# Kernel optimization log

Hardware: AMD Instinct MI355X
Metric: run time of the kernel (lower is better)

## Reference

```python
import jax, jax.numpy as jnp
import numpy as np

NUM_HEADS = 6

def setup_inputs() -> dict:
    key = jax.random.key(0)
    ks = jax.random.split(key, 6)
    B_, N, C = 4096, 64, 192
    nW = 4096
    return {
        "x": jax.random.normal(ks[0], (B_, N, C), dtype=jnp.float32),
        "mask": jax.random.normal(ks[1], (nW, N, N), dtype=jnp.float32),
        "qkv_w": jax.random.normal(ks[2], (3 * C, C), dtype=jnp.float32) * 0.02,
        "qkv_b": jax.random.normal(ks[3], (3 * C,), dtype=jnp.float32) * 0.02,
        "proj_w": jax.random.normal(ks[4], (C, C), dtype=jnp.float32) * 0.02,
        "proj_b": jax.random.normal(ks[5], (C,), dtype=jnp.float32) * 0.02,
    }

def reference(x, mask, qkv_w, qkv_b, proj_w, proj_b):
    B_, N, C = x.shape
    H = NUM_HEADS
    hd = C // H
    scale = hd ** -0.5
    qkv = (x @ qkv_w.T + qkv_b).reshape(B_, N, 3, H, hd)
    qkv = jnp.transpose(qkv, (2, 0, 3, 1, 4))  # [3, B_, H, N, hd]
    q, k, v = qkv[0], qkv[1], qkv[2]
    attn = jnp.einsum('bhnd,bhmd->bhnm', q * scale, k)  # [B_, H, N, N]
    nW = mask.shape[0]
    # additive relative/shift mask broadcast over image batch and heads
    attn = attn.reshape(B_ // nW, nW, H, N, N) + mask[None, :, None, :, :]
    attn = attn.reshape(B_, H, N, N)
    attn = jax.nn.softmax(attn, axis=-1)
    out = jnp.einsum('bhnm,bhmd->bhnd', attn, v)  # [B_, H, N, hd]
    out = jnp.transpose(out, (0, 2, 1, 3)).reshape(B_, N, C)
    return out @ proj_w.T + proj_b
```

## Files before the change

kernel.cpp:

```cpp
#include <hip/hip_runtime.h>
#include <stdint.h>


#define NTOK 64
#define CDIM 192
#define KROW 40
#define VROW 72

#define WS_KV 36864
#define WS_P  110592

typedef __attribute__((ext_vector_type(4))) float f32x4;
typedef __attribute__((ext_vector_type(8))) short bf16x8;

__device__ __forceinline__ short f2bf(float f) {
  union { float f; uint32_t u; } v; v.f = f;
  return (short)(uint16_t)((v.u + 0x7FFFu + ((v.u >> 16) & 1u)) >> 16);
}
__device__ __forceinline__ uint32_t pack2(float a, float b) {
  return (uint32_t)(uint16_t)f2bf(a) | ((uint32_t)(uint16_t)f2bf(b) << 16);
}

__device__ __forceinline__ bf16x8 xpose(uint32_t A0, uint32_t A1,
                                        uint32_t B0, uint32_t B1,
                                        int s0, int s1, int hiSel) {
  uint32_t w[4];
  uint32_t a, b;
  a = (uint32_t)__shfl((int)A0, s0); b = (uint32_t)__shfl((int)B0, s0); w[0] = hiSel ? b : a;
  a = (uint32_t)__shfl((int)A1, s0); b = (uint32_t)__shfl((int)B1, s0); w[1] = hiSel ? b : a;
  a = (uint32_t)__shfl((int)A0, s1); b = (uint32_t)__shfl((int)B0, s1); w[2] = hiSel ? b : a;
  a = (uint32_t)__shfl((int)A1, s1); b = (uint32_t)__shfl((int)B1, s1); w[3] = hiSel ? b : a;
  return *reinterpret_cast<bf16x8*>(w);
}

#define GLOAD16(g, l) __builtin_amdgcn_global_load_lds( \
    (const __attribute__((address_space(1))) void*)(g), \
    (__attribute__((address_space(3))) void*)(l), 16, 0, 0)

__global__ void wconv_kernel(const float* __restrict__ qkv_w,
                             const float* __restrict__ proj_w,
                             short* __restrict__ ws) {
  const int r = blockIdx.x, c = threadIdx.x;
  float val;
  int base, lr;
  if (r < 192) {
    base = (r >> 6) * 12288; lr = r & 63;
    val = qkv_w[r * CDIM + c];
  } else if (r < 576) {
    const int rr = r - 192;
    const int h = (rr % 192) >> 5;
    lr = rr & 31;
    base = WS_KV + h * 12288 + ((rr < 192) ? 0 : 6144);
    val = qkv_w[r * CDIM + c];
  } else {
    const int rr = r - 576;
    base = WS_P + (rr >> 6) * 12288; lr = rr & 63;
    val = proj_w[rr * CDIM + c];
  }
  const int s = c >> 3, lo = c & 7;
  const int sp = (s & 24) | ((s ^ lr) & 7);
  ws[base + lr * CDIM + sp * 8 + lo] = f2bf(val);
}

__device__ __forceinline__ void stage_issue(short* __restrict__ wbuf,
                                            const short* __restrict__ src, int tid) {
  const int w = tid >> 6, lane = tid & 63;
  #pragma unroll
  for (int it = 0; it < 6; ++it) {
    const int cidx = it * 4 + w;
    GLOAD16(src + cidx * 512 + lane * 8, wbuf + cidx * 512);
  }
}

__global__ __launch_bounds__(256, 4)
void winattn_kernel(const float* __restrict__ x, const float* __restrict__ mask,
                    const short* __restrict__ ws,
                    const float* __restrict__ qkv_b, const float* __restrict__ proj_b,
                    float* __restrict__ out) {
  __shared__ __align__(16) short wbuf[64 * CDIM];
  __shared__ __align__(16) short kh[NTOK * KROW];
  __shared__ __align__(16) short vth[32 * VROW];

  const int b    = blockIdx.x;
  const int tid  = threadIdx.x;
  const int lane = tid & 63;
  const int l16  = lane & 15;
  const int g4   = lane >> 4;
  const int m0   = (tid >> 6) * 16;
  const float scale = 0.17677669529663687f;
  const int s0 = (((2 * g4) & 3) << 4) + l16;
  const int s1 = (((2 * g4 + 1) & 3) << 4) + l16;
  const int hiSel = g4 >> 1;

  int soff[6];
  #pragma unroll
  for (int ks = 0; ks < 6; ++ks) {
    const int s = ks * 4 + g4;
    soff[ks] = ((s & 24) | ((s ^ l16) & 7)) << 3;
  }

  stage_issue(wbuf, ws, tid);

  const float* xr = x + (size_t)b * (NTOK * CDIM) + (m0 + l16) * CDIM;
  bf16x8 af[6];
  #pragma unroll
  for (int ks = 0; ks < 6; ++ks) {
    const float4 v0 = *reinterpret_cast<const float4*>(xr + ks * 32 + g4 * 8);
    const float4 v1 = *reinterpret_cast<const float4*>(xr + ks * 32 + g4 * 8 + 4);
    bf16x8 t;
    t[0] = f2bf(v0.x); t[1] = f2bf(v0.y); t[2] = f2bf(v0.z); t[3] = f2bf(v0.w);
    t[4] = f2bf(v1.x); t[5] = f2bf(v1.y); t[6] = f2bf(v1.z); t[7] = f2bf(v1.w);
    af[ks] = t;
  }
  const float* mrowl = mask + (size_t)b * (NTOK * NTOK) + (m0 + l16) * NTOK;
  float4 mreg[4];
  #pragma unroll
  for (int rt = 0; rt < 4; ++rt)
    mreg[rt] = *reinterpret_cast<const float4*>(mrowl + 16 * rt + 4 * g4);

  __syncthreads();

  bf16x8 aq[6];
  #pragma unroll
  for (int c = 0; c < 3; ++c) {
    uint32_t u[4][2];
    #pragma unroll
    for (int lct = 0; lct < 4; ++lct) {
      f32x4 acc = {0.f, 0.f, 0.f, 0.f};
      #pragma unroll
      for (int ks = 0; ks < 6; ++ks) {
        bf16x8 wf = *reinterpret_cast<const bf16x8*>(wbuf + (lct * 16 + l16) * CDIM + soff[ks]);
        acc = __builtin_amdgcn_mfma_f32_16x16x32_bf16(wf, af[ks], acc, 0, 0, 0);
      }
      const float4 bq = *reinterpret_cast<const float4*>(qkv_b + 64 * c + 16 * lct + 4 * g4);
      u[lct][0] = pack2((acc[0] + bq.x) * scale, (acc[1] + bq.y) * scale);
      u[lct][1] = pack2((acc[2] + bq.z) * scale, (acc[3] + bq.w) * scale);
    }
    __syncthreads();
    stage_issue(wbuf, ws + (c < 2 ? (c + 1) * 12288 : WS_KV), tid);
    aq[2 * c]     = xpose(u[0][0], u[0][1], u[1][0], u[1][1], s0, s1, hiSel);
    aq[2 * c + 1] = xpose(u[2][0], u[2][1], u[3][0], u[3][1], s0, s1, hiSel);
    __syncthreads();
  }

  bf16x8 of[6];
  #pragma unroll
  for (int h = 0; h < 6; ++h) {
    #pragma unroll
    for (int lct = 0; lct < 2; ++lct) {
      f32x4 acc = {0.f, 0.f, 0.f, 0.f};
      #pragma unroll
      for (int ks = 0; ks < 6; ++ks) {
        bf16x8 wf = *reinterpret_cast<const bf16x8*>(wbuf + (lct * 16 + l16) * CDIM + soff[ks]);
        acc = __builtin_amdgcn_mfma_f32_16x16x32_bf16(wf, af[ks], acc, 0, 0, 0);
      }
      const float4 bk4 = *reinterpret_cast<const float4*>(qkv_b + 192 + 32 * h + 16 * lct + 4 * g4);
      uint2 kw;
      kw.x = pack2(acc[0] + bk4.x, acc[1] + bk4.y);
      kw.y = pack2(acc[2] + bk4.z, acc[3] + bk4.w);
      *reinterpret_cast<uint2*>(kh + (m0 + l16) * KROW + 16 * lct + 4 * g4) = kw;
    }
    #pragma unroll
    for (int lct = 0; lct < 2; ++lct) {
      f32x4 acc = {0.f, 0.f, 0.f, 0.f};
      #pragma unroll
      for (int ks = 0; ks < 6; ++ks) {
        bf16x8 wf = *reinterpret_cast<const bf16x8*>(wbuf + (32 + lct * 16 + l16) * CDIM + soff[ks]);
        acc = __builtin_amdgcn_mfma_f32_16x16x32_bf16(af[ks], wf, acc, 0, 0, 0);
      }
      const float bv = qkv_b[384 + 32 * h + 16 * lct + l16];
      uint2 vw;
      vw.x = pack2(acc[0] + bv, acc[1] + bv);
      vw.y = pack2(acc[2] + bv, acc[3] + bv);
      *reinterpret_cast<uint2*>(vth + (16 * lct + l16) * VROW + m0 + 4 * g4) = vw;
    }
    __syncthreads();
    stage_issue(wbuf, ws + (h < 5 ? WS_KV + (h + 1) * 12288 : WS_P), tid);

    float p[4][4];
    float rmax = -1e30f;
    #pragma unroll
    for (int rt = 0; rt < 4; ++rt) {
      bf16x8 bk = *reinterpret_cast<const bf16x8*>(kh + (rt * 16 + l16) * KROW + g4 * 8);
      f32x4 z = {0.f, 0.f, 0.f, 0.f};
      f32x4 s = __builtin_amdgcn_mfma_f32_16x16x32_bf16(bk, aq[h], z, 0, 0, 0);
      p[rt][0] = s[0] + mreg[rt].x; p[rt][1] = s[1] + mreg[rt].y;
      p[rt][2] = s[2] + mreg[rt].z; p[rt][3] = s[3] + mreg[rt].w;
      #pragma unroll
      for (int i = 0; i < 4; ++i) rmax = fmaxf(rmax, p[rt][i]);
    }
    rmax = fmaxf(rmax, __shfl_xor(rmax, 16));
    rmax = fmaxf(rmax, __shfl_xor(rmax, 32));
    float rsum = 0.f;
    #pragma unroll
    for (int rt = 0; rt < 4; ++rt)
      #pragma unroll
      for (int i = 0; i < 4; ++i) { p[rt][i] = __expf(p[rt][i] - rmax); rsum += p[rt][i]; }
    rsum += __shfl_xor(rsum, 16);
    rsum += __shfl_xor(rsum, 32);
    const float rinv = 1.f / rsum;

    uint32_t wpk[4][2];
    #pragma unroll
    for (int rt = 0; rt < 4; ++rt) {
      wpk[rt][0] = pack2(p[rt][0] * rinv, p[rt][1] * rinv);
      wpk[rt][1] = pack2(p[rt][2] * rinv, p[rt][3] * rinv);
    }
    bf16x8 bp1 = xpose(wpk[0][0], wpk[0][1], wpk[1][0], wpk[1][1], s0, s1, hiSel);
    bf16x8 bp2 = xpose(wpk[2][0], wpk[2][1], wpk[3][0], wpk[3][1], s0, s1, hiSel);

    uint32_t uo[2][2];
    #pragma unroll
    for (int ct2 = 0; ct2 < 2; ++ct2) {
      const short* vb = vth + (16 * ct2 + l16) * VROW;
      bf16x8 bv1 = *reinterpret_cast<const bf16x8*>(vb + g4 * 8);
      bf16x8 bv2 = *reinterpret_cast<const bf16x8*>(vb + 32 + g4 * 8);
      f32x4 acc = {0.f, 0.f, 0.f, 0.f};
      acc = __builtin_amdgcn_mfma_f32_16x16x32_bf16(bv1, bp1, acc, 0, 0, 0);
      acc = __builtin_amdgcn_mfma_f32_16x16x32_bf16(bv2, bp2, acc, 0, 0, 0);
      uo[ct2][0] = pack2(acc[0], acc[1]);
      uo[ct2][1] = pack2(acc[2], acc[3]);
    }
    of[h] = xpose(uo[0][0], uo[0][1], uo[1][0], uo[1][1], s0, s1, hiSel);

    __syncthreads();
  }

  float* og = out + (size_t)b * (NTOK * CDIM);
  #pragma unroll
  for (int c = 0; c < 3; ++c) {
    f32x4 acc[4];
    #pragma unroll
    for (int lct = 0; lct < 4; ++lct) {
      f32x4 a = {0.f, 0.f, 0.f, 0.f};
      #pragma unroll
      for (int ks = 0; ks < 6; ++ks) {
        bf16x8 wf = *reinterpret_cast<const bf16x8*>(wbuf + (lct * 16 + l16) * CDIM + soff[ks]);
        a = __builtin_amdgcn_mfma_f32_16x16x32_bf16(of[ks], wf, a, 0, 0, 0);
      }
      acc[lct] = a;
    }
    if (c < 2) {
      __syncthreads();
      stage_issue(wbuf, ws + WS_P + (c + 1) * 12288, tid);
    }
    #pragma unroll
    for (int lct = 0; lct < 4; ++lct) {
      const int cc = 64 * c + 16 * lct + l16;
      const float pb = proj_b[cc];
      #pragma unroll
      for (int i = 0; i < 4; ++i)
        og[(m0 + 4 * g4 + i) * CDIM + cc] = acc[lct][i] + pb;
    }
    if (c < 2) __syncthreads();
  }
}

extern "C" void kernel_launch(void* const* d_in, const int* in_sizes, int n_in,
                              void* d_out, int out_size, void* d_ws, size_t ws_size,
                              hipStream_t stream) {
  const float* x      = (const float*)d_in[0];
  const float* mask   = (const float*)d_in[1];
  const float* qkv_w  = (const float*)d_in[2];
  const float* qkv_b  = (const float*)d_in[3];
  const float* proj_w = (const float*)d_in[4];
  const float* proj_b = (const float*)d_in[5];
  float* out = (float*)d_out;

  short* ws = (short*)d_ws;

  wconv_kernel<<<768, 192, 0, stream>>>(qkv_w, proj_w, ws);
  winattn_kernel<<<4096, 256, 0, stream>>>(x, mask, ws, qkv_b, proj_b, out);
}
```

Baseline: 220.0 us.

## Process attention heads in pairs with separate K and V weight stages

Restructures the per-head loop into three iterations that each handle two heads. It stages all K weights for the pair, computes both softmaxes, then stages the V weights and runs both PV products, with K and V sharing one LDS buffer. Weight chunks are re-laid out so each staged 64-row chunk holds K or V for two heads, and the mask is reloaded inside the loop rather than kept in registers. The bf16 conversion also switches to the HIP intrinsic. The intent is fewer barriers and fuller 64-row weight tiles per stage, at the cost of more live registers for the held probabilities and extra mask reloads.

```diff
diff --git a/kernel.cpp b/kernel.cpp
--- a/kernel.cpp
+++ b/kernel.cpp
@@ -1,24 +1,24 @@
 #include <hip/hip_runtime.h>
+#include <hip/hip_bf16.h>
 #include <stdint.h>
 
 
 #define NTOK 64
 #define CDIM 192
-#define KROW 40
-#define VROW 72
-
-#define WS_KV 36864
-#define WS_P  110592
+#define KVROW 72
 
 typedef __attribute__((ext_vector_type(4))) float f32x4;
 typedef __attribute__((ext_vector_type(8))) short bf16x8;
 
 __device__ __forceinline__ short f2bf(float f) {
-  union { float f; uint32_t u; } v; v.f = f;
-  return (short)(uint16_t)((v.u + 0x7FFFu + ((v.u >> 16) & 1u)) >> 16);
+  __hip_bfloat16 h = __float2bfloat16(f);
+  return *reinterpret_cast<short*>(&h);
 }
 __device__ __forceinline__ uint32_t pack2(float a, float b) {
-  return (uint32_t)(uint16_t)f2bf(a) | ((uint32_t)(uint16_t)f2bf(b) << 16);
+  __hip_bfloat162 h2;
+  h2.x = __float2bfloat16(a);
+  h2.y = __float2bfloat16(b);
+  return *reinterpret_cast<uint32_t*>(&h2);
 }
 
 __device__ __forceinline__ bf16x8 xpose(uint32_t A0, uint32_t A1,
@@ -41,25 +41,15 @@
                              const float* __restrict__ proj_w,
                              short* __restrict__ ws) {
   const int r = blockIdx.x, c = threadIdx.x;
+  int chunk, lr;
   float val;
-  int base, lr;
-  if (r < 192) {
-    base = (r >> 6) * 12288; lr = r & 63;
-    val = qkv_w[r * CDIM + c];
-  } else if (r < 576) {
-    const int rr = r - 192;
-    const int h = (rr % 192) >> 5;
-    lr = rr & 31;
-    base = WS_KV + h * 12288 + ((rr < 192) ? 0 : 6144);
-    val = qkv_w[r * CDIM + c];
-  } else {
-    const int rr = r - 576;
-    base = WS_P + (rr >> 6) * 12288; lr = rr & 63;
-    val = proj_w[rr * CDIM + c];
-  }
+  if (r < 192)      { chunk = r >> 6;                     lr = r & 63;          val = qkv_w[r * CDIM + c]; }
+  else if (r < 384) { int q = r - 192; chunk = 3 + 2 * (q >> 6); lr = q & 63;   val = qkv_w[r * CDIM + c]; }
+  else if (r < 576) { int q = r - 384; chunk = 4 + 2 * (q >> 6); lr = q & 63;   val = qkv_w[r * CDIM + c]; }
+  else              { int q = r - 576; chunk = 9 + (q >> 6);     lr = q & 63;   val = proj_w[q * CDIM + c]; }
   const int s = c >> 3, lo = c & 7;
   const int sp = (s & 24) | ((s ^ lr) & 7);
-  ws[base + lr * CDIM + sp * 8 + lo] = f2bf(val);
+  ws[chunk * 12288 + lr * CDIM + sp * 8 + lo] = f2bf(val);
 }
 
 __device__ __forceinline__ void stage_issue(short* __restrict__ wbuf,
@@ -78,8 +68,7 @@
                     const float* __restrict__ qkv_b, const float* __restrict__ proj_b,
                     float* __restrict__ out) {
   __shared__ __align__(16) short wbuf[64 * CDIM];
-  __shared__ __align__(16) short kh[NTOK * KROW];
-  __shared__ __align__(16) short vth[32 * VROW];
+  __shared__ __align__(16) short khv[NTOK * KVROW];
 
   const int b    = blockIdx.x;
   const int tid  = threadIdx.x;
@@ -107,16 +96,12 @@
   for (int ks = 0; ks < 6; ++ks) {
     const float4 v0 = *reinterpret_cast<const float4*>(xr + ks * 32 + g4 * 8);
     const float4 v1 = *reinterpret_cast<const float4*>(xr + ks * 32 + g4 * 8 + 4);
-    bf16x8 t;
-    t[0] = f2bf(v0.x); t[1] = f2bf(v0.y); t[2] = f2bf(v0.z); t[3] = f2bf(v0.w);
-    t[4] = f2bf(v1.x); t[5] = f2bf(v1.y); t[6] = f2bf(v1.z); t[7] = f2bf(v1.w);
-    af[ks] = t;
+    uint32_t t[4];
+    t[0] = pack2(v0.x, v0.y); t[1] = pack2(v0.z, v0.w);
+    t[2] = pack2(v1.x, v1.y); t[3] = pack2(v1.z, v1.w);
+    af[ks] = *reinterpret_cast<bf16x8*>(t);
   }
   const float* mrowl = mask + (size_t)b * (NTOK * NTOK) + (m0 + l16) * NTOK;
-  float4 mreg[4];
-  #pragma unroll
-  for (int rt = 0; rt < 4; ++rt)
-    mreg[rt] = *reinterpret_cast<const float4*>(mrowl + 16 * rt + 4 * g4);
 
   __syncthreads();
 
@@ -137,7 +122,7 @@
       u[lct][1] = pack2((acc[2] + bq.z) * scale, (acc[3] + bq.w) * scale);
     }
     __syncthreads();
-    stage_issue(wbuf, ws + (c < 2 ? (c + 1) * 12288 : WS_KV), tid);
+    stage_issue(wbuf, ws + (c < 2 ? (c + 1) : 3) * 12288, tid);
     aq[2 * c]     = xpose(u[0][0], u[0][1], u[1][0], u[1][1], s0, s1, hiSel);
     aq[2 * c + 1] = xpose(u[2][0], u[2][1], u[3][0], u[3][1], s0, s1, hiSel);
     __syncthreads();
@@ -145,84 +130,98 @@
 
   bf16x8 of[6];
   #pragma unroll
-  for (int h = 0; h < 6; ++h) {
-    #pragma unroll
-    for (int lct = 0; lct < 2; ++lct) {
+  for (int p = 0; p < 3; ++p) {
+    #pragma unroll
+    for (int lct = 0; lct < 4; ++lct) {
       f32x4 acc = {0.f, 0.f, 0.f, 0.f};
       #pragma unroll
       for (int ks = 0; ks < 6; ++ks) {
         bf16x8 wf = *reinterpret_cast<const bf16x8*>(wbuf + (lct * 16 + l16) * CDIM + soff[ks]);
         acc = __builtin_amdgcn_mfma_f32_16x16x32_bf16(wf, af[ks], acc, 0, 0, 0);
       }
-      const float4 bk4 = *reinterpret_cast<const float4*>(qkv_b + 192 + 32 * h + 16 * lct + 4 * g4);
+      const float4 bk4 = *reinterpret_cast<const float4*>(qkv_b + 192 + 64 * p + 16 * lct + 4 * g4);
       uint2 kw;
       kw.x = pack2(acc[0] + bk4.x, acc[1] + bk4.y);
       kw.y = pack2(acc[2] + bk4.z, acc[3] + bk4.w);
-      *reinterpret_cast<uint2*>(kh + (m0 + l16) * KROW + 16 * lct + 4 * g4) = kw;
-    }
-    #pragma unroll
-    for (int lct = 0; lct < 2; ++lct) {
+      *reinterpret_cast<uint2*>(khv + (m0 + l16) * KVROW + 16 * lct + 4 * g4) = kw;
+    }
+    __syncthreads();
+    stage_issue(wbuf, ws + (4 + 2 * p) * 12288, tid);
+
+    float4 mreg[4];
+    #pragma unroll
+    for (int rt = 0; rt < 4; ++rt)
+      mreg[rt] = *reinterpret_cast<const float4*>(mrowl + 16 * rt + 4 * g4);
+
+    bf16x8 bp[2][2];
+    #pragma unroll
+    for (int e = 0; e < 2; ++e) {
+      float pr[4][4];
+      float rmax = -1e30f;
+      #pragma unroll
+      for (int rt = 0; rt < 4; ++rt) {
+        bf16x8 bk = *reinterpret_cast<const bf16x8*>(khv + (rt * 16 + l16) * KVROW + 32 * e + g4 * 8);
+        f32x4 z = {0.f, 0.f, 0.f, 0.f};
+        f32x4 s = __builtin_amdgcn_mfma_f32_16x16x32_bf16(bk, aq[2 * p + e], z, 0, 0, 0);
+        pr[rt][0] = s[0] + mreg[rt].x; pr[rt][1] = s[1] + mreg[rt].y;
+        pr[rt][2] = s[2] + mreg[rt].z; pr[rt][3] = s[3] + mreg[rt].w;
+        #pragma unroll
+        for (int i = 0; i < 4; ++i) rmax = fmaxf(rmax, pr[rt][i]);
+      }
+      rmax = fmaxf(rmax, __shfl_xor(rmax, 16));
+      rmax = fmaxf(rmax, __shfl_xor(rmax, 32));
+      float rsum = 0.f;
+      #pragma unroll
+      for (int rt = 0; rt < 4; ++rt)
+        #pragma unroll
+        for (int i = 0; i < 4; ++i) { pr[rt][i] = __expf(pr[rt][i] - rmax); rsum += pr[rt][i]; }
+      rsum += __shfl_xor(rsum, 16);
+      rsum += __shfl_xor(rsum, 32);
+      const float rinv = 1.f / rsum;
+      uint32_t wpk[4][2];
+      #pragma unroll
+      for (int rt = 0; rt < 4; ++rt) {
+        wpk[rt][0] = pack2(pr[rt][0] * rinv, pr[rt][1] * rinv);
+        wpk[rt][1] = pack2(pr[rt][2] * rinv, pr[rt][3] * rinv);
+      }
+      bp[e][0] = xpose(wpk[0][0], wpk[0][1], wpk[1][0], wpk[1][1], s0, s1, hiSel);
+      bp[e][1] = xpose(wpk[2][0], wpk[2][1], wpk[3][0], wpk[3][1], s0, s1, hiSel);
+    }
+    __syncthreads();
+
+    #pragma unroll
+    for (int lct = 0; lct < 4; ++lct) {
       f32x4 acc = {0.f, 0.f, 0.f, 0.f};
       #pragma unroll
       for (int ks = 0; ks < 6; ++ks) {
-        bf16x8 wf = *reinterpret_cast<const bf16x8*>(wbuf + (32 + lct * 16 + l16) * CDIM + soff[ks]);
+        bf16x8 wf = *reinterpret_cast<const bf16x8*>(wbuf + (lct * 16 + l16) * CDIM + soff[ks]);
         acc = __builtin_amdgcn_mfma_f32_16x16x32_bf16(af[ks], wf, acc, 0, 0, 0);
       }
-      const float bv = qkv_b[384 + 32 * h + 16 * lct + l16];
+      const float bv = qkv_b[384 + 64 * p + 16 * lct + l16];
       uint2 vw;
       vw.x = pack2(acc[0] + bv, acc[1] + bv);
       vw.y = pack2(acc[2] + bv, acc[3] + bv);
-      *reinterpret_cast<uint2*>(vth + (16 * lct + l16) * VROW + m0 + 4 * g4) = vw;
-    }
-    __syncthreads();
-    stage_issue(wbuf, ws + (h < 5 ? WS_KV + (h + 1) * 12288 : WS_P), tid);
-
-    float p[4][4];
-    float rmax = -1e30f;
-    #pragma unroll
-    for (int rt = 0; rt < 4; ++rt) {
-      bf16x8 bk = *reinterpret_cast<const bf16x8*>(kh + (rt * 16 + l16) * KROW + g4 * 8);
-      f32x4 z = {0.f, 0.f, 0.f, 0.f};
-      f32x4 s = __builtin_amdgcn_mfma_f32_16x16x32_bf16(bk, aq[h], z, 0, 0, 0);
-      p[rt][0] = s[0] + mreg[rt].x; p[rt][1] = s[1] + mreg[rt].y;
-      p[rt][2] = s[2] + mreg[rt].z; p[rt][3] = s[3] + mreg[rt].w;
-      #pragma unroll
-      for (int i = 0; i < 4; ++i) rmax = fmaxf(rmax, p[rt][i]);
-    }
-    rmax = fmaxf(rmax, __shfl_xor(rmax, 16));
-    rmax = fmaxf(rmax, __shfl_xor(rmax, 32));
-    float rsum = 0.f;
-    #pragma unroll
-    for (int rt = 0; rt < 4; ++rt)
-      #pragma unroll
-      for (int i = 0; i < 4; ++i) { p[rt][i] = __expf(p[rt][i] - rmax); rsum += p[rt][i]; }
-    rsum += __shfl_xor(rsum, 16);
-    rsum += __shfl_xor(rsum, 32);
-    const float rinv = 1.f / rsum;
-
-    uint32_t wpk[4][2];
-    #pragma unroll
-    for (int rt = 0; rt < 4; ++rt) {
-      wpk[rt][0] = pack2(p[rt][0] * rinv, p[rt][1] * rinv);
-      wpk[rt][1] = pack2(p[rt][2] * rinv, p[rt][3] * rinv);
-    }
-    bf16x8 bp1 = xpose(wpk[0][0], wpk[0][1], wpk[1][0], wpk[1][1], s0, s1, hiSel);
-    bf16x8 bp2 = xpose(wpk[2][0], wpk[2][1], wpk[3][0], wpk[3][1], s0, s1, hiSel);
-
-    uint32_t uo[2][2];
-    #pragma unroll
-    for (int ct2 = 0; ct2 < 2; ++ct2) {
-      const short* vb = vth + (16 * ct2 + l16) * VROW;
-      bf16x8 bv1 = *reinterpret_cast<const bf16x8*>(vb + g4 * 8);
-      bf16x8 bv2 = *reinterpret_cast<const bf16x8*>(vb + 32 + g4 * 8);
-      f32x4 acc = {0.f, 0.f, 0.f, 0.f};
-      acc = __builtin_amdgcn_mfma_f32_16x16x32_bf16(bv1, bp1, acc, 0, 0, 0);
-      acc = __builtin_amdgcn_mfma_f32_16x16x32_bf16(bv2, bp2, acc, 0, 0, 0);
-      uo[ct2][0] = pack2(acc[0], acc[1]);
-      uo[ct2][1] = pack2(acc[2], acc[3]);
-    }
-    of[h] = xpose(uo[0][0], uo[0][1], uo[1][0], uo[1][1], s0, s1, hiSel);
-
+      *reinterpret_cast<uint2*>(khv + (16 * lct + l16) * KVROW + m0 + 4 * g4) = vw;
+    }
+    __syncthreads();
+    stage_issue(wbuf, ws + (p < 2 ? (5 + 2 * p) : 9) * 12288, tid);
+
+    #pragma unroll
+    for (int e = 0; e < 2; ++e) {
+      uint32_t uo[2][2];
+      #pragma unroll
+      for (int ct2 = 0; ct2 < 2; ++ct2) {
+        const short* vb = khv + (32 * e + 16 * ct2 + l16) * KVROW;
+        bf16x8 bv1 = *reinterpret_cast<const bf16x8*>(vb + g4 * 8);
+        bf16x8 bv2 = *reinterpret_cast<const bf16x8*>(vb + 32 + g4 * 8);
+        f32x4 acc = {0.f, 0.f, 0.f, 0.f};
+        acc = __builtin_amdgcn_mfma_f32_16x16x32_bf16(bv1, bp[e][0], acc, 0, 0, 0);
+        acc = __builtin_amdgcn_mfma_f32_16x16x32_bf16(bv2, bp[e][1], acc, 0, 0, 0);
+        uo[ct2][0] = pack2(acc[0], acc[1]);
+        uo[ct2][1] = pack2(acc[2], acc[3]);
+      }
+      of[2 * p + e] = xpose(uo[0][0], uo[0][1], uo[1][0], uo[1][1], s0, s1, hiSel);
+    }
     __syncthreads();
   }
 
@@ -242,7 +241,7 @@
     }
     if (c < 2) {
       __syncthreads();
-      stage_issue(wbuf, ws + WS_P + (c + 1) * 12288, tid);
+      stage_issue(wbuf, ws + (10 + c) * 12288, tid);
     }
     #pragma unroll
     for (int lct = 0; lct < 4; ++lct) {
```

Result: slower. 243.4 us (+10.7%).
